# Kernel optimization log

Measured on AMD Instinct MI355X. Metric: run time of the kernel, lower is better.

Reference implementation:

```python
import jax, jax.numpy as jnp
import numpy as np

N_HEADS = 16
HIDDEN = 1024
DIM = 1024
SCALE = float(HIDDEN ** (-5))  # faithful to source (likely-intended -0.5 is NOT used)


def setup_inputs() -> dict:
    key = jax.random.key(0)
    ks = jax.random.split(key, 5)
    b, s = 2, 2048
    x = jax.random.normal(ks[0], (b, s, DIM), dtype=jnp.float32)
    mask = jnp.ones((b, s), dtype=jnp.int32)
    # nn.Linear weights are [out_features, in_features]
    w_std = DIM ** -0.5
    Wq = jax.random.normal(ks[1], (HIDDEN, DIM), dtype=jnp.float32) * w_std
    Wk = jax.random.normal(ks[2], (HIDDEN, DIM), dtype=jnp.float32) * w_std
    Wv = jax.random.normal(ks[3], (HIDDEN, DIM), dtype=jnp.float32) * w_std
    Wo = jax.random.normal(ks[4], (DIM, HIDDEN), dtype=jnp.float32) * w_std
    return {"x": x, "mask": mask, "Wq": Wq, "Wk": Wk, "Wv": Wv, "Wo": Wo}


def reference(x, mask, Wq, Wk, Wv, Wo):
    b, s, _ = x.shape
    hd = HIDDEN // N_HEADS
    # projections (Linear: y = x @ W.T), split heads: b i (h d) -> b i h d
    q = (x @ Wq.T).reshape(b, s, N_HEADS, hd)
    k = (x @ Wk.T).reshape(b, s, N_HEADS, hd)
    v = (x @ Wv.T).reshape(b, s, N_HEADS, hd)
    # scores: h b i j
    scores = jnp.einsum("bihd,bjhd->hbij", q * SCALE, k)
    big_neg = -jnp.finfo(scores.dtype).max
    # 2D mask: b j -> broadcast over h and i (repeat 'b i -> h b 1 i')
    m = mask.astype(bool)[None, :, None, :]  # [1, b, 1, j]
    scores = jnp.where(m, scores, big_neg)
    attn = jax.nn.softmax(scores, axis=-1)  # [h, b, i, j]
    out = jnp.einsum("hbij,bjhd->bihd", attn, v).reshape(b, s, HIDDEN)
    out = out @ Wo.T
    return out, attn
```

## Files before the change

kernel.cpp:

```cpp
#include <hip/hip_runtime.h>


#define DIMN 1024
#define SEQ  2048
#define BATCH 2

typedef float vfloat4 __attribute__((ext_vector_type(4)));

#define WS_XSUM  0
#define WS_CNT   2048
#define WS_TMP   2052
#define WS_OVEC  4100

__global__ void k_reduce_x(const float* __restrict__ x,
                           const int* __restrict__ mask,
                           float* __restrict__ ws) {
    const int b = blockIdx.y;
    const int tid = threadIdx.x;
    const int j0 = blockIdx.x * 16;
    const float* xb = x + (size_t)b * SEQ * DIMN;

    float a0 = 0.f, a1 = 0.f, a2 = 0.f, a3 = 0.f;
    for (int j = j0; j < j0 + 16; ++j) {
        if (mask[b * SEQ + j]) {
            const float* row = xb + (size_t)j * DIMN;
            a0 += row[tid];
            a1 += row[tid + 256];
            a2 += row[tid + 512];
            a3 += row[tid + 768];
        }
    }
    atomicAdd(&ws[WS_XSUM + b * DIMN + tid],       a0);
    atomicAdd(&ws[WS_XSUM + b * DIMN + tid + 256], a1);
    atomicAdd(&ws[WS_XSUM + b * DIMN + tid + 512], a2);
    atomicAdd(&ws[WS_XSUM + b * DIMN + tid + 768], a3);

    if (tid < 16) {
        float s = (mask[b * SEQ + j0 + tid] != 0) ? 1.f : 0.f;
        s += __shfl_down(s, 8, 64);
        s += __shfl_down(s, 4, 64);
        s += __shfl_down(s, 2, 64);
        s += __shfl_down(s, 1, 64);
        if (tid == 0) atomicAdd(&ws[WS_CNT + b], s);
    }
}

__global__ void k_matvec(const float* __restrict__ W,
                         const float* __restrict__ vin,
                         float* __restrict__ vout,
                         const float* __restrict__ cnt,
                         int divide) {
    const int gw = (blockIdx.x * 256 + threadIdx.x) >> 6;
    const int lane = threadIdx.x & 63;
    const int b = gw >> 10;
    const int r = gw & 1023;
    const float* wr = W + (size_t)r * DIMN;
    const float* vb = vin + b * DIMN;
    float s = 0.f;
#pragma unroll
    for (int k = 0; k < DIMN / 64; ++k)
        s += wr[lane + k * 64] * vb[lane + k * 64];
#pragma unroll
    for (int off = 32; off; off >>= 1) s += __shfl_down(s, off, 64);
    if (lane == 0) {
        if (divide) s /= cnt[b];
        vout[b * DIMN + r] = s;
    }
}

__global__ void k_megafill(float* __restrict__ out, float* __restrict__ attn,
                           const int* __restrict__ mask,
                           const float* __restrict__ ws) {
    const int tid = threadIdx.x;
    if (blockIdx.x < 256) {
        const float* ovec = ws + WS_OVEC;
#pragma unroll 4
        for (int f = blockIdx.x * 256 + tid; f < (1 << 20); f += 256 * 256) {
            const int b  = f >> 19;
            const int d4 = f & 255;
            vfloat4 v = ((const vfloat4*)(ovec + b * DIMN))[d4];
            __builtin_nontemporal_store(v, ((vfloat4*)out) + f);
        }
    } else {
        const float r0 = 1.0f / ws[WS_CNT];
        const float r1 = 1.0f / ws[WS_CNT + 1];
        const int4* m4 = (const int4*)mask;
        const int stride = 8192 * 256;
#pragma unroll 4
        for (int f = (blockIdx.x - 256) * 256 + tid; f < (1 << 25); f += stride) {
            const int j4 = f & 511;
            const int b  = (f >> 20) & 1;
            const int4 m = m4[b * 512 + j4];
            const float r = b ? r1 : r0;
            vfloat4 v;
            v.x = m.x ? r : 0.f;
            v.y = m.y ? r : 0.f;
            v.z = m.z ? r : 0.f;
            v.w = m.w ? r : 0.f;
            __builtin_nontemporal_store(v, ((vfloat4*)attn) + f);
        }
    }
}

extern "C" void kernel_launch(void* const* d_in, const int* in_sizes, int n_in,
                              void* d_out, int out_size, void* d_ws, size_t ws_size,
                              hipStream_t stream) {
    const float* x    = (const float*)d_in[0];
    const int*   mask = (const int*)d_in[1];
    const float* Wv   = (const float*)d_in[4];
    const float* Wo   = (const float*)d_in[5];

    float* ws   = (float*)d_ws;
    float* out  = (float*)d_out;
    float* attn = out + (size_t)BATCH * SEQ * DIMN;

    (void)hipMemsetAsync(d_ws, 0, (WS_CNT + 2) * sizeof(float), stream);

    dim3 rg(128, BATCH);
    k_reduce_x<<<rg, 256, 0, stream>>>(x, mask, ws);
    k_matvec<<<512, 256, 0, stream>>>(Wv, ws + WS_XSUM, ws + WS_TMP,  ws + WS_CNT, 1);
    k_matvec<<<512, 256, 0, stream>>>(Wo, ws + WS_TMP,  ws + WS_OVEC, ws + WS_CNT, 0);
    k_megafill<<<8448, 256, 0, stream>>>(out, attn, mask, ws);
}
```

Measured before the change: 604.9 us.

## Fuse reduction, matvecs and fills into one cooperative kernel with grid syncs

```diff
diff --git a/kernel.cpp b/kernel.cpp
--- a/kernel.cpp
+++ b/kernel.cpp
@@ -1,93 +1,117 @@
 #include <hip/hip_runtime.h>
+#include <hip/hip_cooperative_groups.h>
+
+namespace cg = cooperative_groups;
 
 
 #define DIMN 1024
 #define SEQ  2048
 #define BATCH 2
 
-typedef float vfloat4 __attribute__((ext_vector_type(4)));
-
 #define WS_XSUM  0
 #define WS_CNT   2048
 #define WS_TMP   2052
 #define WS_OVEC  4100
 
-__global__ void k_reduce_x(const float* __restrict__ x,
-                           const int* __restrict__ mask,
-                           float* __restrict__ ws) {
-    const int b = blockIdx.y;
-    const int tid = threadIdx.x;
-    const int j0 = blockIdx.x * 16;
-    const float* xb = x + (size_t)b * SEQ * DIMN;
+typedef float vfloat4 __attribute__((ext_vector_type(4)));
 
-    float a0 = 0.f, a1 = 0.f, a2 = 0.f, a3 = 0.f;
-    for (int j = j0; j < j0 + 16; ++j) {
-        if (mask[b * SEQ + j]) {
-            const float* row = xb + (size_t)j * DIMN;
-            a0 += row[tid];
-            a1 += row[tid + 256];
-            a2 += row[tid + 512];
-            a3 += row[tid + 768];
+__global__ __launch_bounds__(256, 4)
+void k_fused(const float* __restrict__ x,
+             const int* __restrict__ mask,
+             const float* __restrict__ Wv,
+             const float* __restrict__ Wo,
+             float* __restrict__ ws,
+             float* __restrict__ out,
+             float* __restrict__ attn) {
+    cg::grid_group grid = cg::this_grid();
+    const int tid  = threadIdx.x;
+    const int gtid = blockIdx.x * 256 + tid;
+    const int lane = tid & 63;
+    const int wave = tid >> 6;
+
+    if (gtid < WS_CNT + 2) ws[gtid] = 0.f;
+    grid.sync();
+
+    {
+        const int row0 = blockIdx.x * 4;
+        const int b = row0 >> 11;
+        float a0 = 0.f, a1 = 0.f, a2 = 0.f, a3 = 0.f;
+#pragma unroll
+        for (int rr = 0; rr < 4; ++rr) {
+            const int row = row0 + rr;
+            if (mask[row]) {
+                const float* r = x + (size_t)row * DIMN;
+                a0 += r[tid];
+                a1 += r[tid + 256];
+                a2 += r[tid + 512];
+                a3 += r[tid + 768];
+            }
+        }
+        atomicAdd(&ws[WS_XSUM + b * DIMN + tid],       a0);
+        atomicAdd(&ws[WS_XSUM + b * DIMN + tid + 256], a1);
+        atomicAdd(&ws[WS_XSUM + b * DIMN + tid + 512], a2);
+        atomicAdd(&ws[WS_XSUM + b * DIMN + tid + 768], a3);
+        if (tid < 4) {
+            float s = (mask[row0 + tid] != 0) ? 1.f : 0.f;
+            s += __shfl_down(s, 2, 64);
+            s += __shfl_down(s, 1, 64);
+            if (tid == 0) atomicAdd(&ws[WS_CNT + b], s);
         }
     }
-    atomicAdd(&ws[WS_XSUM + b * DIMN + tid],       a0);
-    atomicAdd(&ws[WS_XSUM + b * DIMN + tid + 256], a1);
-    atomicAdd(&ws[WS_XSUM + b * DIMN + tid + 512], a2);
-    atomicAdd(&ws[WS_XSUM + b * DIMN + tid + 768], a3);
+    grid.sync();
 
-    if (tid < 16) {
-        float s = (mask[b * SEQ + j0 + tid] != 0) ? 1.f : 0.f;
-        s += __shfl_down(s, 8, 64);
-        s += __shfl_down(s, 4, 64);
-        s += __shfl_down(s, 2, 64);
-        s += __shfl_down(s, 1, 64);
-        if (tid == 0) atomicAdd(&ws[WS_CNT + b], s);
+    {
+        const int gw = blockIdx.x * 4 + wave;
+        if (gw < 2048) {
+            const int b = gw >> 10;
+            const int r = gw & 1023;
+            const float* wr = Wv + (size_t)r * DIMN;
+            const float* vb = ws + WS_XSUM + b * DIMN;
+            float s = 0.f;
+#pragma unroll
+            for (int k = 0; k < DIMN / 64; ++k)
+                s += wr[lane + k * 64] * vb[lane + k * 64];
+#pragma unroll
+            for (int off = 32; off; off >>= 1) s += __shfl_down(s, off, 64);
+            if (lane == 0) ws[WS_TMP + b * DIMN + r] = s / ws[WS_CNT + b];
+        }
     }
-}
+    grid.sync();
 
-__global__ void k_matvec(const float* __restrict__ W,
-                         const float* __restrict__ vin,
-                         float* __restrict__ vout,
-                         const float* __restrict__ cnt,
-                         int divide) {
-    const int gw = (blockIdx.x * 256 + threadIdx.x) >> 6;
-    const int lane = threadIdx.x & 63;
-    const int b = gw >> 10;
-    const int r = gw & 1023;
-    const float* wr = W + (size_t)r * DIMN;
-    const float* vb = vin + b * DIMN;
-    float s = 0.f;
+    {
+        const int gw = blockIdx.x * 4 + wave;
+        if (gw < 2048) {
+            const int b = gw >> 10;
+            const int r = gw & 1023;
+            const float* wr = Wo + (size_t)r * DIMN;
+            const float* vb = ws + WS_TMP + b * DIMN;
+            float s = 0.f;
 #pragma unroll
-    for (int k = 0; k < DIMN / 64; ++k)
-        s += wr[lane + k * 64] * vb[lane + k * 64];
+            for (int k = 0; k < DIMN / 64; ++k)
+                s += wr[lane + k * 64] * vb[lane + k * 64];
 #pragma unroll
-    for (int off = 32; off; off >>= 1) s += __shfl_down(s, off, 64);
-    if (lane == 0) {
-        if (divide) s /= cnt[b];
-        vout[b * DIMN + r] = s;
+            for (int off = 32; off; off >>= 1) s += __shfl_down(s, off, 64);
+            if (lane == 0) ws[WS_OVEC + b * DIMN + r] = s;
+        }
     }
-}
+    grid.sync();
 
-__global__ void k_megafill(float* __restrict__ out, float* __restrict__ attn,
-                           const int* __restrict__ mask,
-                           const float* __restrict__ ws) {
-    const int tid = threadIdx.x;
-    if (blockIdx.x < 256) {
-        const float* ovec = ws + WS_OVEC;
-#pragma unroll 4
-        for (int f = blockIdx.x * 256 + tid; f < (1 << 20); f += 256 * 256) {
+    {
+        const float r0 = 1.0f / ws[WS_CNT];
+        const float r1 = 1.0f / ws[WS_CNT + 1];
+        const vfloat4* ovec4 = (const vfloat4*)(ws + WS_OVEC);
+        vfloat4* out4  = (vfloat4*)out;
+        vfloat4* attn4 = (vfloat4*)attn;
+        const int4* m4 = (const int4*)mask;
+        const int NT = 1024 * 256;
+
+#pragma unroll
+        for (int f = gtid; f < (1 << 20); f += NT) {
             const int b  = f >> 19;
             const int d4 = f & 255;
-            vfloat4 v = ((const vfloat4*)(ovec + b * DIMN))[d4];
-            __builtin_nontemporal_store(v, ((vfloat4*)out) + f);
+            out4[f] = ovec4[b * 256 + d4];
         }
-    } else {
-        const float r0 = 1.0f / ws[WS_CNT];
-        const float r1 = 1.0f / ws[WS_CNT + 1];
-        const int4* m4 = (const int4*)mask;
-        const int stride = 8192 * 256;
-#pragma unroll 4
-        for (int f = (blockIdx.x - 256) * 256 + tid; f < (1 << 25); f += stride) {
+        for (int f = gtid; f < (1 << 25); f += NT) {
             const int j4 = f & 511;
             const int b  = (f >> 20) & 1;
             const int4 m = m4[b * 512 + j4];
@@ -97,7 +121,7 @@
             v.y = m.y ? r : 0.f;
             v.z = m.z ? r : 0.f;
             v.w = m.w ? r : 0.f;
-            __builtin_nontemporal_store(v, ((vfloat4*)attn) + f);
+            attn4[f] = v;
         }
     }
 }
@@ -114,11 +138,8 @@
     float* out  = (float*)d_out;
     float* attn = out + (size_t)BATCH * SEQ * DIMN;
 
-    (void)hipMemsetAsync(d_ws, 0, (WS_CNT + 2) * sizeof(float), stream);
-
-    dim3 rg(128, BATCH);
-    k_reduce_x<<<rg, 256, 0, stream>>>(x, mask, ws);
-    k_matvec<<<512, 256, 0, stream>>>(Wv, ws + WS_XSUM, ws + WS_TMP,  ws + WS_CNT, 1);
-    k_matvec<<<512, 256, 0, stream>>>(Wo, ws + WS_TMP,  ws + WS_OVEC, ws + WS_CNT, 0);
-    k_megafill<<<8448, 256, 0, stream>>>(out, attn, mask, ws);
+    void* args[] = {(void*)&x, (void*)&mask, (void*)&Wv, (void*)&Wo,
+                    (void*)&ws, (void*)&out, (void*)&attn};
+    (void)hipLaunchCooperativeKernel((void*)k_fused, dim3(1024), dim3(256),
+                                     args, 0, stream);
 }
```

Result: slower. 912.0 us (+50.8%).
